# Kernel optimization log

Hardware: AMD Instinct MI355X
Metric: run time of the kernel (lower is better)

Reference implementation:

```python
import jax, jax.numpy as jnp
import numpy as np

D_MODEL = 1024
NHEAD = 16
D_K = D_MODEL // NHEAD


def setup_inputs() -> dict:
    key = jax.random.key(0)
    ks = jax.random.split(key, 10)
    B, S = 2, 2048
    x = jax.random.normal(ks[0], (B, S, D_MODEL), dtype=jnp.float32)
    # sorted 1-D coordinate grid in [0,1], shape [S,1,1] so coords.shape[1]==1
    coords = jnp.sort(jax.random.uniform(ks[1], (S, 1, 1), dtype=jnp.float32), axis=0)
    sc = 1.0 / np.sqrt(D_MODEL)
    Wq = jax.random.normal(ks[2], (D_MODEL, D_MODEL), dtype=jnp.float32) * sc
    bq = jnp.zeros((D_MODEL,), jnp.float32)
    Wk = jax.random.normal(ks[3], (D_MODEL, D_MODEL), dtype=jnp.float32) * sc
    bk = jnp.zeros((D_MODEL,), jnp.float32)
    Wv = jax.random.normal(ks[4], (D_MODEL, D_MODEL), dtype=jnp.float32) * sc
    bv = jnp.zeros((D_MODEL,), jnp.float32)
    Wo = jax.random.normal(ks[5], (D_MODEL, D_MODEL), dtype=jnp.float32) * sc
    bo = jnp.zeros((D_MODEL,), jnp.float32)
    return {"x": x, "coords": coords, "Wq": Wq, "bq": bq, "Wk": Wk, "bk": bk,
            "Wv": Wv, "bv": bv, "Wo": Wo, "bo": bo}


def _split_heads(t):  # [B,S,D] -> [B,H,S,Dk]
    B, S, _ = t.shape
    return t.reshape(B, S, NHEAD, D_K).transpose(0, 2, 1, 3)


def reference(x, coords, Wq, bq, Wk, bk, Wv, bv, Wo, bo):
    B, S, _ = x.shape
    Q = _split_heads(x @ Wq.T + bq)
    K = _split_heads(x @ Wk.T + bk)
    V = _split_heads(x @ Wv.T + bv)

    scale = jnp.sqrt(jnp.float32(D_K))
    scores = jnp.einsum('bhld,bhsd->bhls', Q, K) / scale  # [B,H,S,S]

    # trapezoidal quadrature weights from coord grid: [S-1] -> broadcast shapes
    dc = jnp.abs(coords[1:] - coords[:-1]).reshape(1, 1, 1, S - 1)  # key-axis

    # custom trapezoidal softmax
    e = jnp.exp(scores - jnp.max(scores, axis=-1, keepdims=True))
    denom = jnp.sum(0.5 * dc * (e[..., 1:] + e[..., :-1]), axis=-1, keepdims=True)
    aw = e / denom  # [B,H,S,S]

    dcv = dc.reshape(1, 1, S - 1, 1)  # value-axis weighting
    o1 = jnp.einsum('bhls,bhsd->bhld', aw[..., 1:], dcv * V[:, :, 1:, :])
    o2 = jnp.einsum('bhls,bhsd->bhld', aw[..., :-1], dcv * V[:, :, :-1, :])
    out = 0.5 * (o1 + o2)  # [B,H,S,Dk]

    out = out.transpose(0, 2, 1, 3).reshape(B, S, D_MODEL)
    return out @ Wo.T + bo
```

## Files before the change

kernel.cpp:

```cpp
#include <hip/hip_runtime.h>

#define DM 1024
#define NHEAD 16
#define DK 64
#define QLD 3072

typedef short bf16x8 __attribute__((ext_vector_type(8)));
typedef float f32x4 __attribute__((ext_vector_type(4)));

__device__ __forceinline__ unsigned short f2bf(float f) {
  union { float f; unsigned u; } v; v.f = f;
  return (unsigned short)((v.u + 0x7fffu + ((v.u >> 16) & 1u)) >> 16);
}
__device__ __forceinline__ float bf2f(unsigned short h) {
  union { unsigned u; float f; } v; v.u = ((unsigned)h) << 16; return v.f;
}
__device__ __forceinline__ float fexp2(float x) {
  float r; asm("v_exp_f32 %0, %1" : "=v"(r) : "v"(x)); return r;
}

__device__ __forceinline__ void gld16(const void* g, void* l) {
  __builtin_amdgcn_global_load_lds((const __attribute__((address_space(1))) void*)g,
                                   (__attribute__((address_space(3))) void*)l, 16, 0, 0);
}

__device__ __forceinline__ int kappa(int p) {
  return (p & 32) + (((p & 7) >> 2) << 4) + (((p >> 3) & 3) << 2) + (p & 3);
}

__global__ void k_prep(const float* __restrict__ x, const float* __restrict__ Wq,
                       const float* __restrict__ Wk, const float* __restrict__ Wv,
                       const float* __restrict__ Wo, const float* __restrict__ bq,
                       const float* __restrict__ bk, const float* __restrict__ bv,
                       const float* __restrict__ coords,
                       unsigned short* __restrict__ xb, unsigned short* __restrict__ Wcat,
                       unsigned short* __restrict__ Wob, float* __restrict__ bcat,
                       float* __restrict__ tw, unsigned short* __restrict__ twb,
                       int M, int S, float QS) {
  const int nx = M * DM / 4;
  const int nw = DM * DM / 4;
  const int total = nx + 4 * nw;
  int gid = blockIdx.x * 256 + threadIdx.x;

  auto conv4 = [&](const float* src, unsigned short* dst, int idx, float sc) {
    float4 v = *(const float4*)(src + idx * 4);
    ushort4 o;
    o.x = f2bf(v.x * sc); o.y = f2bf(v.y * sc);
    o.z = f2bf(v.z * sc); o.w = f2bf(v.w * sc);
    *(ushort4*)(dst + idx * 4) = o;
  };

  if (gid < nx) { conv4(x, xb, gid, 1.0f); return; }
  if (gid < nx + nw) { conv4(Wq, Wcat, gid - nx, QS); return; }
  if (gid < nx + 2 * nw) { conv4(Wk, Wcat + DM * DM, gid - nx - nw, 1.0f); return; }
  if (gid < nx + 3 * nw) { conv4(Wv, Wcat + 2 * DM * DM, gid - nx - 2 * nw, 1.0f); return; }
  if (gid < total) { conv4(Wo, Wob, gid - nx - 3 * nw, 1.0f); return; }

  int r = gid - total;
  if (r < 3 * DM) {
    float v = (r < DM) ? bq[r] * QS : (r < 2 * DM ? bk[r - DM] : bv[r - 2 * DM]);
    bcat[r] = v;
    return;
  }
  r -= 3 * DM;
  if (r < S) {
    auto twval = [&](int k) {
      float a = (k > 0)     ? fabsf(coords[k] - coords[k - 1]) : 0.f;
      float b = (k < S - 1) ? fabsf(coords[k + 1] - coords[k]) : 0.f;
      return 0.5f * (a + b);
    };
    tw[r] = twval(r);
    int key = (r & ~63) + kappa(r & 63);
    twb[r] = f2bf(twval(key));
  }
}

#define BM 128
#define BN 128
#define BKK 64

template<int OUTF32>
__global__ __launch_bounds__(256)
void gemm_bt(const unsigned short* __restrict__ A, const unsigned short* __restrict__ B,
             const float* __restrict__ bias, void* __restrict__ C,
             int M, int N, int K, int ldc) {
  __shared__ __align__(16) unsigned short sA[2][BM * BKK];
  __shared__ __align__(16) unsigned short sB[2][BN * BKK];
  const int tid = threadIdx.x;
  const int lane = tid & 63;
  const int wid = tid >> 6;
  const int rr = lane & 15, g = lane >> 4;
  const int nbn = N / BN;
  const int cpx = gridDim.x >> 3;
  const int bid = ((gridDim.x & 7) == 0) ? (blockIdx.x & 7) * cpx + (blockIdx.x >> 3)
                                         : blockIdx.x;
  const int bm = bid / nbn, bn = bid % nbn;
  const int wr = wid >> 1, wc = wid & 1;
  const int nkt = K / BKK;

  const unsigned short* Abase = A + (size_t)bm * BM * K;
  const unsigned short* Bbase = B + (size_t)bn * BN * K;

  auto stage = [&](int buf, int kt) {
#pragma unroll
    for (int j = 0; j < 4; ++j) {
      int o = j * 256 + tid;
      int row = o >> 3;
      int cb = ((o & 7) * 16) ^ ((row & 7) << 4);
      gld16((const char*)(Abase + (size_t)row * K + kt * BKK) + cb, &sA[buf][o * 8]);
      gld16((const char*)(Bbase + (size_t)row * K + kt * BKK) + cb, &sB[buf][o * 8]);
    }
  };

  f32x4 acc[4][4] = {};
  stage(0, 0);
  int cur = 0;
  const int sw = (rr & 7) << 4;
  for (int kt = 0; kt < nkt; ++kt) {
    __syncthreads();
    if (kt + 1 < nkt) stage(cur ^ 1, kt + 1);
    const char* a0 = (const char*)&sA[cur][(wr * 64) * BKK];
    const char* b0 = (const char*)&sB[cur][(wc * 64) * BKK];
#pragma unroll
    for (int kk = 0; kk < 2; ++kk) {
      const int co = (kk * 64 + g * 16);
      bf16x8 af[4], bfr[4];
#pragma unroll
      for (int m = 0; m < 4; ++m)
        af[m] = *(const bf16x8*)(a0 + (m * 16 + rr) * 128 + (co ^ sw));
#pragma unroll
      for (int n = 0; n < 4; ++n)
        bfr[n] = *(const bf16x8*)(b0 + (n * 16 + rr) * 128 + (co ^ sw));
      __builtin_amdgcn_s_setprio(1);
#pragma unroll
      for (int m = 0; m < 4; ++m)
#pragma unroll
        for (int n = 0; n < 4; ++n)
          acc[m][n] = __builtin_amdgcn_mfma_f32_16x16x32_bf16(af[m], bfr[n], acc[m][n], 0, 0, 0);
      __builtin_amdgcn_s_setprio(0);
    }
    cur ^= 1;
  }

  const int crow0 = bm * BM + wr * 64;
  const int ccol0 = bn * BN + wc * 64;
#pragma unroll
  for (int n = 0; n < 4; ++n) {
    const int col = ccol0 + n * 16 + rr;
    const float bn_ = bias ? bias[col] : 0.f;
#pragma unroll
    for (int m = 0; m < 4; ++m)
#pragma unroll
      for (int r = 0; r < 4; ++r) {
        const int row = crow0 + m * 16 + g * 4 + r;
        float v = acc[m][n][r] + bn_;
        if (OUTF32) ((float*)C)[(size_t)row * ldc + col] = v;
        else ((unsigned short*)C)[(size_t)row * ldc + col] = f2bf(v);
      }
  }
}

__global__ __launch_bounds__(256)
void k_transpose(const unsigned short* __restrict__ V, const float* __restrict__ tw,
                 unsigned short* __restrict__ Vt, int S, int ld) {
  __shared__ __align__(16) unsigned short t[64][72];
  __shared__ float tws[64];
  const int nst = S / 64;
  int st = blockIdx.x % nst;
  int bh = blockIdx.x / nst;
  int h = bh & (NHEAD - 1), b = bh / NHEAD;
  const unsigned short* src = V + ((size_t)b * S + st * 64) * ld + h * DK;
  unsigned short* dst = Vt + (size_t)bh * DK * S + st * 64;
  int tid = threadIdx.x;
  if (tid < 64) tws[tid] = tw[st * 64 + tid];
#pragma unroll
  for (int i = 0; i < 2; ++i) {
    int r = i * 32 + (tid >> 3);
    int c = (tid & 7) * 8;
    *(uint4*)&t[r][c] = *(const uint4*)&src[(size_t)r * ld + c];
  }
  __syncthreads();
#pragma unroll
  for (int i = 0; i < 2; ++i) {
    int d = i * 32 + (tid >> 3);
    int p0 = (tid & 7) * 8;
    unsigned short tmp[8];
#pragma unroll
    for (int j = 0; j < 8; ++j) {
      int kl = kappa(p0 + j);
      tmp[j] = f2bf(bf2f(t[kl][d]) * tws[kl]);
    }
    *(uint4*)&dst[(size_t)d * S + p0] = *(const uint4*)&tmp[0];
  }
}

__global__ __launch_bounds__(256)
void k_attn(const unsigned short* __restrict__ QKV, const unsigned short* __restrict__ Vt,
            const unsigned short* __restrict__ twb, unsigned short* __restrict__ O, int S) {
  __shared__ __align__(16) unsigned short sK[2][128 * 64];
  __shared__ __align__(16) unsigned short sV[2][64 * 128];
  const int tid = threadIdx.x, lane = tid & 63, wid = tid >> 6;
  const int rr = lane & 15, g = lane >> 4;
  const int nqt = S / 128;
  const int cpx = gridDim.x >> 3;
  const int swz = (blockIdx.x & 7) * cpx + (blockIdx.x >> 3);
  const int qt = swz % nqt;
  const int bh = swz / nqt;
  const int h = bh & (NHEAD - 1), b = bh / NHEAD;

  const unsigned short* Qbase = QKV + ((size_t)b * S + qt * 128 + wid * 32) * QLD + h * DK;
  const unsigned short* Kbase = QKV + (size_t)b * S * QLD + DM + h * DK;
  const unsigned short* Vbase = Vt + (size_t)bh * DK * S;

  bf16x8 aq[2][2];
#pragma unroll
  for (int qm = 0; qm < 2; ++qm) {
    aq[qm][0] = *(const bf16x8*)&Qbase[(size_t)(qm * 16 + rr) * QLD + g * 8];
    aq[qm][1] = *(const bf16x8*)&Qbase[(size_t)(qm * 16 + rr) * QLD + 32 + g * 8];
  }

  f32x4 acc[2][5] = {};
  const f32x4 z0 = {};

  auto stage = [&](int buf, int kt) {
#pragma unroll
    for (int j = 0; j < 4; ++j) {
      int o = j * 256 + tid;
      int row = o >> 3;
      int cb = ((o & 7) * 16) ^ ((row & 7) << 4);
      gld16((const char*)(Kbase + (size_t)(kt * 128 + row) * QLD) + cb, &sK[buf][o * 8]);
    }
#pragma unroll
    for (int j = 0; j < 4; ++j) {
      int o = j * 256 + tid;
      int row = o >> 4;
      int cb = ((o & 15) * 16) ^ ((row & 7) << 4);
      gld16((const char*)(Vbase + (size_t)row * S + kt * 128) + cb, &sV[buf][o * 8]);
    }
  };

  stage(0, 0);
  int cur = 0;
  const int nkt = S / 128;
  for (int kt = 0; kt < nkt; ++kt) {
    __syncthreads();
    if (kt + 1 < nkt) stage(cur ^ 1, kt + 1);

#pragma unroll
    for (int half = 0; half < 2; ++half) {
      f32x4 s[2][4];
#pragma unroll
      for (int f = 0; f < 4; ++f) {
        const int row = half * 64 + f * 16 + rr;
        const int swr = (rr & 7) << 4;
        bf16x8 kA0 = *(const bf16x8*)((const char*)&sK[cur][row * 64] + ((g * 16) ^ swr));
        bf16x8 kA1 = *(const bf16x8*)((const char*)&sK[cur][row * 64] + ((64 + g * 16) ^ swr));
        __builtin_amdgcn_s_setprio(1);
#pragma unroll
        for (int qm = 0; qm < 2; ++qm) {
          f32x4 z = __builtin_amdgcn_mfma_f32_16x16x32_bf16(kA0, aq[qm][0], z0, 0, 0, 0);
          s[qm][f] = __builtin_amdgcn_mfma_f32_16x16x32_bf16(kA1, aq[qm][1], z, 0, 0, 0);
        }
        __builtin_amdgcn_s_setprio(0);
      }

#pragma unroll
      for (int qm = 0; qm < 2; ++qm)
#pragma unroll
        for (int f = 0; f < 4; ++f)
#pragma unroll
          for (int r = 0; r < 4; ++r)
            s[qm][f][r] = fexp2(s[qm][f][r]);

      bf16x8 pa[2][2];
#pragma unroll
      for (int qm = 0; qm < 2; ++qm)
#pragma unroll
        for (int kk = 0; kk < 2; ++kk) {
          union { bf16x8 v; unsigned u[4]; } pk;
          asm("v_cvt_pk_bf16_f32 %0, %1, %2" : "=v"(pk.u[0]) : "v"(s[qm][2*kk][0]),   "v"(s[qm][2*kk][1]));
          asm("v_cvt_pk_bf16_f32 %0, %1, %2" : "=v"(pk.u[1]) : "v"(s[qm][2*kk][2]),   "v"(s[qm][2*kk][3]));
          asm("v_cvt_pk_bf16_f32 %0, %1, %2" : "=v"(pk.u[2]) : "v"(s[qm][2*kk+1][0]), "v"(s[qm][2*kk+1][1]));
          asm("v_cvt_pk_bf16_f32 %0, %1, %2" : "=v"(pk.u[3]) : "v"(s[qm][2*kk+1][2]), "v"(s[qm][2*kk+1][3]));
          pa[qm][kk] = pk.v;
        }

      bf16x8 tw0 = *(const bf16x8*)&twb[kt * 128 + half * 64 + g * 8];
      bf16x8 tw1 = *(const bf16x8*)&twb[kt * 128 + half * 64 + 32 + g * 8];

#pragma unroll
      for (int kk = 0; kk < 2; ++kk) {
        __builtin_amdgcn_s_setprio(1);
#pragma unroll
        for (int n = 0; n < 4; ++n) {
          const int vrow = n * 16 + rr;
          const int cb = (half * 128 + kk * 64 + g * 16) ^ ((vrow & 7) << 4);
          bf16x8 bv = *(const bf16x8*)((const char*)&sV[cur][vrow * 128] + cb);
#pragma unroll
          for (int qm = 0; qm < 2; ++qm)
            acc[qm][n] = __builtin_amdgcn_mfma_f32_16x16x32_bf16(pa[qm][kk], bv, acc[qm][n], 0, 0, 0);
        }
#pragma unroll
        for (int qm = 0; qm < 2; ++qm)
          acc[qm][4] = __builtin_amdgcn_mfma_f32_16x16x32_bf16(pa[qm][kk], kk ? tw1 : tw0, acc[qm][4], 0, 0, 0);
        __builtin_amdgcn_s_setprio(0);
      }
    }
    cur ^= 1;
  }

  unsigned short* Ob = O + ((size_t)b * S + qt * 128 + wid * 32) * DM + h * DK;
#pragma unroll
  for (int qm = 0; qm < 2; ++qm)
#pragma unroll
    for (int n = 0; n < 4; ++n)
#pragma unroll
      for (int r = 0; r < 4; ++r) {
        const int q = qm * 16 + g * 4 + r;
        const int d = n * 16 + rr;
        Ob[(size_t)q * DM + d] = f2bf(acc[qm][n][r] / acc[qm][4][r]);
      }
}

extern "C" void kernel_launch(void* const* d_in, const int* in_sizes, int n_in,
                              void* d_out, int out_size, void* d_ws, size_t ws_size,
                              hipStream_t stream) {
  const float* x      = (const float*)d_in[0];
  const float* coords = (const float*)d_in[1];
  const float* Wq = (const float*)d_in[2];
  const float* bq = (const float*)d_in[3];
  const float* Wk = (const float*)d_in[4];
  const float* bk = (const float*)d_in[5];
  const float* Wv = (const float*)d_in[6];
  const float* bv = (const float*)d_in[7];
  const float* Wo = (const float*)d_in[8];
  const float* bo = (const float*)d_in[9];

  const int S = in_sizes[1];
  const int B = in_sizes[0] / (S * DM);
  const int M = B * S;
  const float QS = 0.18033688011112042f;

  char* w = (char*)d_ws;
  size_t off = 0;
  unsigned short* xb   = (unsigned short*)(w + off); off += (size_t)M * DM * 2;
  unsigned short* Wcat = (unsigned short*)(w + off); off += (size_t)3 * DM * DM * 2;
  unsigned short* Wob  = (unsigned short*)(w + off); off += (size_t)DM * DM * 2;
  unsigned short* QKVb = (unsigned short*)(w + off); off += (size_t)M * QLD * 2;
  unsigned short* Vtb  = (unsigned short*)(w + off); off += (size_t)M * DM * 2;
  float* tw  = (float*)(w + off); off += (size_t)S * 4;
  unsigned short* twb = (unsigned short*)(w + off); off += (size_t)S * 2;
  float* bcat = (float*)(w + off); off += (size_t)3 * DM * 4;
  unsigned short* Ob = xb;
  (void)ws_size; (void)n_in; (void)out_size;

  {
    int nx = M * DM / 4, nw = DM * DM / 4;
    int total = nx + 4 * nw;
    int tail = 3 * DM + S;
    int gridp = total / 256 + (tail + 255) / 256;
    k_prep<<<gridp, 256, 0, stream>>>(x, Wq, Wk, Wv, Wo, bq, bk, bv, coords,
                                      xb, Wcat, Wob, bcat, tw, twb, M, S, QS);
  }

  gemm_bt<0><<<(M / BM) * (3 * DM / BN), 256, 0, stream>>>(xb, Wcat, bcat, QKVb, M, 3 * DM, DM, QLD);

  k_transpose<<<B * NHEAD * (S / 64), 256, 0, stream>>>(QKVb + 2 * DM, tw, Vtb, S, QLD);
  k_attn<<<B * NHEAD * (S / 128), 256, 0, stream>>>(QKVb, Vtb, twb, Ob, S);

  gemm_bt<1><<<(M / BM) * (DM / BN), 256, 0, stream>>>(Ob, Wob, bo, d_out, M, DM, DM, DM);
}
```

Measured before the change: 123.5 us.

## Stage bf16 GEMM epilogue through LDS and batch QK^T before exp in attention

The bf16-output GEMM epilogue now writes the tile into shared memory, which reuses the merged A/B staging buffer, and then emits coalesced 16-byte row stores instead of scattered 2-byte stores. In the attention kernel, both halves of the QK^T score MFMAs are computed before any exponentials, giving more independent MFMA and exp work to interleave. The cost is two extra barriers in the GEMM epilogue and higher register pressure in the attention loop, which may lower occupancy.

New measurement: 113.1 us. 1.09x faster.

```diff
diff --git a/kernel.cpp b/kernel.cpp
--- a/kernel.cpp
+++ b/kernel.cpp
@@ -84,8 +84,7 @@
 void gemm_bt(const unsigned short* __restrict__ A, const unsigned short* __restrict__ B,
              const float* __restrict__ bias, void* __restrict__ C,
              int M, int N, int K, int ldc) {
-  __shared__ __align__(16) unsigned short sA[2][BM * BKK];
-  __shared__ __align__(16) unsigned short sB[2][BN * BKK];
+  __shared__ __align__(16) unsigned short smem[4][BM * BKK];
   const int tid = threadIdx.x;
   const int lane = tid & 63;
   const int wid = tid >> 6;
@@ -107,8 +106,8 @@
       int o = j * 256 + tid;
       int row = o >> 3;
       int cb = ((o & 7) * 16) ^ ((row & 7) << 4);
-      gld16((const char*)(Abase + (size_t)row * K + kt * BKK) + cb, &sA[buf][o * 8]);
-      gld16((const char*)(Bbase + (size_t)row * K + kt * BKK) + cb, &sB[buf][o * 8]);
+      gld16((const char*)(Abase + (size_t)row * K + kt * BKK) + cb, &smem[buf][o * 8]);
+      gld16((const char*)(Bbase + (size_t)row * K + kt * BKK) + cb, &smem[2 + buf][o * 8]);
     }
   };
 
@@ -119,8 +118,8 @@
   for (int kt = 0; kt < nkt; ++kt) {
     __syncthreads();
     if (kt + 1 < nkt) stage(cur ^ 1, kt + 1);
-    const char* a0 = (const char*)&sA[cur][(wr * 64) * BKK];
-    const char* b0 = (const char*)&sB[cur][(wc * 64) * BKK];
+    const char* a0 = (const char*)&smem[cur][(wr * 64) * BKK];
+    const char* b0 = (const char*)&smem[2 + cur][(wc * 64) * BKK];
 #pragma unroll
     for (int kk = 0; kk < 2; ++kk) {
       const int co = (kk * 64 + g * 16);
@@ -144,19 +143,42 @@
 
   const int crow0 = bm * BM + wr * 64;
   const int ccol0 = bn * BN + wc * 64;
-#pragma unroll
-  for (int n = 0; n < 4; ++n) {
-    const int col = ccol0 + n * 16 + rr;
-    const float bn_ = bias ? bias[col] : 0.f;
-#pragma unroll
-    for (int m = 0; m < 4; ++m)
-#pragma unroll
-      for (int r = 0; r < 4; ++r) {
-        const int row = crow0 + m * 16 + g * 4 + r;
-        float v = acc[m][n][r] + bn_;
-        if (OUTF32) ((float*)C)[(size_t)row * ldc + col] = v;
-        else ((unsigned short*)C)[(size_t)row * ldc + col] = f2bf(v);
-      }
+  if (OUTF32) {
+#pragma unroll
+    for (int n = 0; n < 4; ++n) {
+      const int col = ccol0 + n * 16 + rr;
+      const float bn_ = bias ? bias[col] : 0.f;
+#pragma unroll
+      for (int m = 0; m < 4; ++m)
+#pragma unroll
+        for (int r = 0; r < 4; ++r) {
+          const int row = crow0 + m * 16 + g * 4 + r;
+          ((float*)C)[(size_t)row * ldc + col] = acc[m][n][r] + bn_;
+        }
+    }
+  } else {
+    unsigned short* L = &smem[0][0];
+    __syncthreads();
+#pragma unroll
+    for (int n = 0; n < 4; ++n) {
+      const float bn_ = bias ? bias[ccol0 + n * 16 + rr] : 0.f;
+#pragma unroll
+      for (int m = 0; m < 4; ++m)
+#pragma unroll
+        for (int r = 0; r < 4; ++r)
+          L[(wr * 64 + m * 16 + g * 4 + r) * 136 + wc * 64 + n * 16 + rr] =
+              f2bf(acc[m][n][r] + bn_);
+    }
+    __syncthreads();
+    unsigned short* Cb = (unsigned short*)C + (size_t)(bm * BM) * ldc + bn * BN;
+#pragma unroll
+    for (int i = 0; i < 8; ++i) {
+      int o = i * 256 + tid;
+      int row = o >> 4;
+      int cc = (o & 15) * 8;
+      uint4 v = *(const uint4*)&L[row * 136 + cc];
+      *(uint4*)&Cb[(size_t)row * ldc + cc] = v;
+    }
   }
 }
 
@@ -242,46 +264,51 @@
   stage(0, 0);
   int cur = 0;
   const int nkt = S / 128;
+  const int swr = (rr & 7) << 4;
   for (int kt = 0; kt < nkt; ++kt) {
     __syncthreads();
     if (kt + 1 < nkt) stage(cur ^ 1, kt + 1);
 
+    f32x4 s[2][2][4];
 #pragma unroll
     for (int half = 0; half < 2; ++half) {
-      f32x4 s[2][4];
 #pragma unroll
       for (int f = 0; f < 4; ++f) {
         const int row = half * 64 + f * 16 + rr;
-        const int swr = (rr & 7) << 4;
         bf16x8 kA0 = *(const bf16x8*)((const char*)&sK[cur][row * 64] + ((g * 16) ^ swr));
         bf16x8 kA1 = *(const bf16x8*)((const char*)&sK[cur][row * 64] + ((64 + g * 16) ^ swr));
         __builtin_amdgcn_s_setprio(1);
 #pragma unroll
         for (int qm = 0; qm < 2; ++qm) {
           f32x4 z = __builtin_amdgcn_mfma_f32_16x16x32_bf16(kA0, aq[qm][0], z0, 0, 0, 0);
-          s[qm][f] = __builtin_amdgcn_mfma_f32_16x16x32_bf16(kA1, aq[qm][1], z, 0, 0, 0);
+          s[half][qm][f] = __builtin_amdgcn_mfma_f32_16x16x32_bf16(kA1, aq[qm][1], z, 0, 0, 0);
         }
         __builtin_amdgcn_s_setprio(0);
       }
-
+    }
+
+#pragma unroll
+    for (int half = 0; half < 2; ++half)
 #pragma unroll
       for (int qm = 0; qm < 2; ++qm)
 #pragma unroll
         for (int f = 0; f < 4; ++f)
 #pragma unroll
           for (int r = 0; r < 4; ++r)
-            s[qm][f][r] = fexp2(s[qm][f][r]);
-
+            s[half][qm][f][r] = fexp2(s[half][qm][f][r]);
+
+#pragma unroll
+    for (int half = 0; half < 2; ++half) {
       bf16x8 pa[2][2];
 #pragma unroll
       for (int qm = 0; qm < 2; ++qm)
 #pragma unroll
         for (int kk = 0; kk < 2; ++kk) {
           union { bf16x8 v; unsigned u[4]; } pk;
-          asm("v_cvt_pk_bf16_f32 %0, %1, %2" : "=v"(pk.u[0]) : "v"(s[qm][2*kk][0]),   "v"(s[qm][2*kk][1]));
-          asm("v_cvt_pk_bf16_f32 %0, %1, %2" : "=v"(pk.u[1]) : "v"(s[qm][2*kk][2]),   "v"(s[qm][2*kk][3]));
-          asm("v_cvt_pk_bf16_f32 %0, %1, %2" : "=v"(pk.u[2]) : "v"(s[qm][2*kk+1][0]), "v"(s[qm][2*kk+1][1]));
-          asm("v_cvt_pk_bf16_f32 %0, %1, %2" : "=v"(pk.u[3]) : "v"(s[qm][2*kk+1][2]), "v"(s[qm][2*kk+1][3]));
+          asm("v_cvt_pk_bf16_f32 %0, %1, %2" : "=v"(pk.u[0]) : "v"(s[half][qm][2*kk][0]),   "v"(s[half][qm][2*kk][1]));
+          asm("v_cvt_pk_bf16_f32 %0, %1, %2" : "=v"(pk.u[1]) : "v"(s[half][qm][2*kk][2]),   "v"(s[half][qm][2*kk][3]));
+          asm("v_cvt_pk_bf16_f32 %0, %1, %2" : "=v"(pk.u[2]) : "v"(s[half][qm][2*kk+1][0]), "v"(s[half][qm][2*kk+1][1]));
+          asm("v_cvt_pk_bf16_f32 %0, %1, %2" : "=v"(pk.u[3]) : "v"(s[half][qm][2*kk+1][2]), "v"(s[half][qm][2*kk+1][3]));
           pa[qm][kk] = pk.v;
         }
 
```
